# Kernel optimization log

Measured on AMD Instinct MI355X. Metric: run time of the kernel, lower is better.

## Reference

```python
import jax, jax.numpy as jnp
import numpy as np

N_NODES = 10000
N_EDGES = 100000
F_NODE = 128
F_EDGE = 16
HEADS = 8
OUT_CH = 128  # per-head channels in PyG TransformerConv
HC = HEADS * OUT_CH


def setup_inputs() -> dict:
    key = jax.random.key(0)
    ks = jax.random.split(key, 12)
    sN = 1.0 / np.sqrt(F_NODE)
    sE = 1.0 / np.sqrt(F_EDGE)
    return {
        "x": jax.random.normal(ks[0], (N_NODES, F_NODE), dtype=jnp.float32),
        "edge_attr": jax.random.normal(ks[1], (N_EDGES, F_EDGE), dtype=jnp.float32),
        "edge_index": jax.random.randint(ks[2], (2, N_EDGES), 0, N_NODES, dtype=jnp.int32),
        "Wq": jax.random.normal(ks[3], (F_NODE, HC), dtype=jnp.float32) * sN,
        "bq": jnp.zeros((HC,), dtype=jnp.float32),
        "Wk": jax.random.normal(ks[4], (F_NODE, HC), dtype=jnp.float32) * sN,
        "bk": jnp.zeros((HC,), dtype=jnp.float32),
        "Wv": jax.random.normal(ks[5], (F_NODE, HC), dtype=jnp.float32) * sN,
        "bv": jnp.zeros((HC,), dtype=jnp.float32),
        "We": jax.random.normal(ks[6], (F_EDGE, HC), dtype=jnp.float32) * sE,  # lin_edge has no bias in PyG
        "Wskip": jax.random.normal(ks[7], (F_NODE, OUT_CH), dtype=jnp.float32) * sN,
        "bskip": jnp.zeros((OUT_CH,), dtype=jnp.float32),
        "Wd": jax.random.normal(ks[8], (OUT_CH, 1), dtype=jnp.float32) * (1.0 / np.sqrt(OUT_CH)),
        "bd": jnp.zeros((1,), dtype=jnp.float32),
    }


def reference(x, edge_attr, edge_index, Wq, bq, Wk, bk, Wv, bv, We, Wskip, bskip, Wd, bd):
    N = x.shape[0]
    src, dst = edge_index[0], edge_index[1]  # messages flow src -> dst

    q = (x @ Wq + bq).reshape(N, HEADS, OUT_CH)
    k = (x @ Wk + bk).reshape(N, HEADS, OUT_CH)
    v = (x @ Wv + bv).reshape(N, HEADS, OUT_CH)
    e = (edge_attr @ We).reshape(-1, HEADS, OUT_CH)  # [E, H, C]

    k_j = k[src] + e                        # [E, H, C]
    alpha = jnp.einsum("ehc,ehc->eh", q[dst], k_j) / np.sqrt(OUT_CH)  # [E, H]

    # segment softmax over destination node
    m = jax.ops.segment_max(alpha, dst, num_segments=N)   # [N, H]
    a = jnp.exp(alpha - m[dst])
    s = jax.ops.segment_sum(a, dst, num_segments=N)       # [N, H]
    alpha_n = a / (s[dst] + 1e-16)                        # [E, H]

    msg = (v[src] + e) * alpha_n[:, :, None]              # [E, H, C]
    out = jax.ops.segment_sum(msg, dst, num_segments=N)   # [N, H, C]

    out = out.mean(axis=1)                                # concat=False -> head average, [N, C]
    out = out + x @ Wskip + bskip                         # root/skip connection
    out = jax.nn.relu(out)
    # dropout is identity at inference
    pooled = out.sum(axis=0)                              # [C]
    return pooled @ Wd + bd                               # [1]
```

## Files before the change

### kernel.cpp

```cpp
#include <hip/hip_runtime.h>

#define N_NODES 10000
#define N_EDGES 100000
#define F_NODE 128
#define HEADS 8
#define HC 1024
#define NCOLS2 2432
#define NB2 (NCOLS2 / 128)
#define SLOT_CAP 48

typedef __attribute__((ext_vector_type(8))) short bf16x8;
typedef __attribute__((ext_vector_type(4))) float f32x4;
typedef __attribute__((ext_vector_type(2))) float f32x2;

__device__ __forceinline__ void atomAddF(float* p, float v) {
    unsafeAtomicAdd(p, v);
}
__device__ __forceinline__ unsigned short f2bf(float f) {
    union { float f; unsigned u; } c; c.f = f;
    unsigned u = c.u + 0x7fffu + ((c.u >> 16) & 1u);
    return (unsigned short)(u >> 16);
}
__device__ __forceinline__ float bLo(unsigned x) {
    union { unsigned u; float f; } c; c.u = x << 16; return c.f;
}
__device__ __forceinline__ float bHi(unsigned x) {
    union { unsigned u; float f; } c; c.u = x & 0xffff0000u; return c.f;
}
__device__ __forceinline__ float bf2f(unsigned short u) {
    union { unsigned u; float f; } c; c.u = ((unsigned)u) << 16; return c.f;
}
__device__ __forceinline__ unsigned pk4fp8(unsigned a, unsigned b) {
    int w = __builtin_amdgcn_cvt_pk_fp8_f32(bLo(a), bHi(a), 0, false);
    w = __builtin_amdgcn_cvt_pk_fp8_f32(bLo(b), bHi(b), w, true);
    return (unsigned)w;
}
__device__ __forceinline__ void dq16v(uint4 q, f32x2* f) {
    f[0] = __builtin_amdgcn_cvt_pk_f32_fp8(q.x, false);
    f[1] = __builtin_amdgcn_cvt_pk_f32_fp8(q.x, true);
    f[2] = __builtin_amdgcn_cvt_pk_f32_fp8(q.y, false);
    f[3] = __builtin_amdgcn_cvt_pk_f32_fp8(q.y, true);
    f[4] = __builtin_amdgcn_cvt_pk_f32_fp8(q.z, false);
    f[5] = __builtin_amdgcn_cvt_pk_f32_fp8(q.z, true);
    f[6] = __builtin_amdgcn_cvt_pk_f32_fp8(q.w, false);
    f[7] = __builtin_amdgcn_cvt_pk_f32_fp8(q.w, true);
}
__device__ __forceinline__ void edge_accum2(
    uint4 xq4, uint4 vq4, float2 eav, float svv, bool valid,
    const f32x2* gf2, float qwx, float qwy, float du_r, float scale,
    float& s_reg, float& t0, float& t1, f32x2* va2) {
    f32x2 dac;
    dac.x = eav.x * qwx;
    dac.y = eav.y * qwy;
    f32x2 p;
    p = __builtin_amdgcn_cvt_pk_f32_fp8(xq4.x, false); dac += gf2[0] * p;
    p = __builtin_amdgcn_cvt_pk_f32_fp8(xq4.x, true);  dac += gf2[1] * p;
    p = __builtin_amdgcn_cvt_pk_f32_fp8(xq4.y, false); dac += gf2[2] * p;
    p = __builtin_amdgcn_cvt_pk_f32_fp8(xq4.y, true);  dac += gf2[3] * p;
    p = __builtin_amdgcn_cvt_pk_f32_fp8(xq4.z, false); dac += gf2[4] * p;
    p = __builtin_amdgcn_cvt_pk_f32_fp8(xq4.z, true);  dac += gf2[5] * p;
    p = __builtin_amdgcn_cvt_pk_f32_fp8(xq4.w, false); dac += gf2[6] * p;
    p = __builtin_amdgcn_cvt_pk_f32_fp8(xq4.w, true);  dac += gf2[7] * p;
    float d = dac.x + dac.y;
    d += __shfl_xor(d, 1); d += __shfl_xor(d, 2); d += __shfl_xor(d, 4);
    float a = __expf((d + du_r + svv) * scale);
    a = valid ? a : 0.f;
    s_reg += a;
    t0 += a * eav.x; t1 += a * eav.y;
    f32x2 av; av.x = a; av.y = a;
    p = __builtin_amdgcn_cvt_pk_f32_fp8(vq4.x, false); va2[0] += av * p;
    p = __builtin_amdgcn_cvt_pk_f32_fp8(vq4.x, true);  va2[1] += av * p;
    p = __builtin_amdgcn_cvt_pk_f32_fp8(vq4.y, false); va2[2] += av * p;
    p = __builtin_amdgcn_cvt_pk_f32_fp8(vq4.y, true);  va2[3] += av * p;
    p = __builtin_amdgcn_cvt_pk_f32_fp8(vq4.z, false); va2[4] += av * p;
    p = __builtin_amdgcn_cvt_pk_f32_fp8(vq4.z, true);  va2[5] += av * p;
    p = __builtin_amdgcn_cvt_pk_f32_fp8(vq4.w, false); va2[6] += av * p;
    p = __builtin_amdgcn_cvt_pk_f32_fp8(vq4.w, true);  va2[7] += av * p;
}

#define PREP_A 1250
#define PREP_B (PREP_A + NCOLS2 / 2)
#define PREP_C (PREP_B + 10)
#define PREP_D (PREP_C + 64)
__global__ __launch_bounds__(256) void prep_all(
    const float* __restrict__ x, unsigned short* __restrict__ xb,
    unsigned* __restrict__ xf8, const int* __restrict__ ei,
    int* __restrict__ cnt, int2* __restrict__ slots,
    const float* __restrict__ Wq, const float* __restrict__ Wk,
    const float* __restrict__ Wv, const float* __restrict__ Wskip,
    const float* __restrict__ We, const float* __restrict__ bq,
    const float* __restrict__ bk, const float* __restrict__ bv,
    const float* __restrict__ bskip, unsigned short* __restrict__ wt,
    float* __restrict__ bias, unsigned short* __restrict__ w2t) {
    __shared__ float wesh[2][128];
    __shared__ float wqsh[64][129];
    int tid = threadIdx.x;
    if (blockIdx.x < PREP_A) {
        int i = blockIdx.x * 256 + tid;
        float4 f = ((const float4*)x)[i];
        ushort4 o;
        o.x = f2bf(f.x); o.y = f2bf(f.y); o.z = f2bf(f.z); o.w = f2bf(f.w);
        ((ushort4*)xb)[i] = o;
        int w = __builtin_amdgcn_cvt_pk_fp8_f32(f.x, f.y, 0, false);
        w = __builtin_amdgcn_cvt_pk_fp8_f32(f.z, f.w, w, true);
        xf8[i] = (unsigned)w;
        if (i < N_EDGES) {
            int src = ei[i];
            int dst = ei[N_EDGES + i];
            int pos = atomicAdd(&cnt[dst], 1);
            if (pos < SLOT_CAP) slots[(size_t)dst * SLOT_CAP + pos] = make_int2(src, i);
        }
    } else if (blockIdx.x < PREP_B) {
        int bi = blockIdx.x - PREP_A;
        int cid = tid >> 7, d = tid & 127;
        int n = 2 * bi + cid;
        bool panel = (n < 1024) || (n >= 2176 && n < 2304);
        if (panel) {
            int h = (n < 1024) ? (n >> 7) : ((n - 2176) >> 4);
            if (n < 1024) {
                int f2 = n & 127;
                wesh[cid][d] = Wk[(size_t)f2 * HC + h * 128 + d];
            } else {
                int f = (n - 2176) & 15;
                wesh[cid][d] = We[(size_t)f * HC + h * 128 + d];
            }
            float s = 0.f;
            int c_t = tid & 63, r_t = tid >> 6;
            #pragma unroll 2
            for (int half = 0; half < 2; ++half) {
                #pragma unroll
                for (int rr = 0; rr < 32; ++rr) {
                    int r = rr * 4 + r_t;
                    wqsh[c_t][r] = Wq[(size_t)r * HC + h * 128 + half * 64 + c_t];
                }
                __syncthreads();
                #pragma unroll 16
                for (int cc = 0; cc < 64; ++cc)
                    s += wqsh[cc][d] * wesh[cid][half * 64 + cc];
                __syncthreads();
            }
            wt[(size_t)n * 128 + d] = f2bf(s);
        } else {
            float val;
            if (n < 2048) {
                val = Wv[(size_t)d * HC + (n - 1024)];
            } else if (n < 2176) {
                val = Wskip[(size_t)d * 128 + (n - 2048)];
            } else if (n < 2312) {
                int h = n - 2304;
                wesh[cid][d] = bk[h * 128 + d];
                __syncthreads();
                const float* wq = Wq + (size_t)d * HC + h * 128;
                float s = 0.f;
                #pragma unroll
                for (int c = 0; c < 128; ++c) s += wq[c] * wesh[cid][c];
                val = s;
            } else if (n < 2320) {
                int h = n - 2312;
                wesh[cid][d] = bq[h * 128 + d];
                __syncthreads();
                const float* wk = Wk + (size_t)d * HC + h * 128;
                float s = 0.f;
                #pragma unroll
                for (int c = 0; c < 128; ++c) s += wk[c] * wesh[cid][c];
                val = s;
            } else {
                val = 0.f;
            }
            wt[(size_t)n * 128 + d] = f2bf(val);
        }
    } else if (blockIdx.x < PREP_C) {
        int n = (blockIdx.x - PREP_B) * 256 + tid;
        if (n >= NCOLS2) return;
        float val;
        if (n < 1024) val = 0.f;
        else if (n < 2048) val = bv[n - 1024];
        else if (n < 2176) val = bskip[n - 2048];
        else if (n < 2304) {
            int hf = n - 2176, h = hf >> 4, f = hf & 15;
            float s = 0.f;
            for (int c = 0; c < 128; ++c)
                s += bq[h * 128 + c] * We[(size_t)f * HC + h * 128 + c];
            val = s;
        } else if (n < 2312) {
            int h = n - 2304;
            float s = 0.f;
            for (int c = 0; c < 128; ++c) s += bq[h * 128 + c] * bk[h * 128 + c];
            val = s;
        } else val = 0.f;
        bias[n] = val;
    } else {
        int c = (blockIdx.x - PREP_C) * 2 + (tid >> 7);
        int d = tid & 127;
        int h = d >> 4, f = d & 15;
        w2t[(size_t)c * 128 + d] = f2bf(We[(size_t)f * HC + h * 128 + c] * 0.125f);
    }
}

__global__ __launch_bounds__(256) void gemm_mfma(
    const unsigned short* __restrict__ xb, const unsigned short* __restrict__ wt,
    const float* __restrict__ bias, unsigned char* __restrict__ xgf8,
    unsigned char* __restrict__ vf8, unsigned short* __restrict__ sqb,
    float* __restrict__ du, float* __restrict__ sv) {
    __shared__ unsigned short lds[32768];
    unsigned short* ldsA = lds;
    unsigned short* ldsB = lds + 16384;
    int tid = threadIdx.x;
    int n0 = blockIdx.x * 128, m0 = blockIdx.y * 128;
    int w = tid >> 6, lane = tid & 63;
    int wm = (w >> 1) * 64, wn = (w & 1) * 64;
    int quad = lane >> 4, l16 = lane & 15;

    #pragma unroll
    for (int j = 0; j < 8; ++j) {
        int idx = j * 256 + tid;
        int kg = idx >> 7, r = idx & 127;
        unsigned short* dstA = ldsA + (size_t)(j * 256 + w * 64) * 8;
        __builtin_amdgcn_global_load_lds(
            (const unsigned int*)(xb + (size_t)(m0 + r) * 128 + kg * 8),
            (unsigned int*)dstA, 16, 0, 0);
    }
    #pragma unroll
    for (int j = 0; j < 8; ++j) {
        int idx = j * 256 + tid;
        int kg = idx >> 7, r = idx & 127;
        unsigned short* dstB = ldsB + (size_t)(j * 256 + w * 64) * 8;
        __builtin_amdgcn_global_load_lds(
            (const unsigned int*)(wt + (size_t)(n0 + r) * 128 + kg * 8),
            (unsigned int*)dstB, 16, 0, 0);
    }
    __syncthreads();

    f32x4 acc[4][4];
    #pragma unroll
    for (int i = 0; i < 4; ++i)
        #pragma unroll
        for (int j = 0; j < 4; ++j) acc[i][j] = (f32x4){0.f, 0.f, 0.f, 0.f};

    #pragma unroll
    for (int ks = 0; ks < 128; ks += 32) {
        int kb = (ks >> 3) + quad;
        bf16x8 a[4], b[4];
        #pragma unroll
        for (int mt = 0; mt < 4; ++mt)
            a[mt] = *(const bf16x8*)(ldsA + (size_t)kb * 1024 + (wm + mt * 16 + l16) * 8);
        #pragma unroll
        for (int nt = 0; nt < 4; ++nt)
            b[nt] = *(const bf16x8*)(ldsB + (size_t)kb * 1024 + (wn + nt * 16 + l16) * 8);
        #pragma unroll
        for (int mt = 0; mt < 4; ++mt)
            #pragma unroll
            for (int nt = 0; nt < 4; ++nt)
                acc[mt][nt] = __builtin_amdgcn_mfma_f32_16x16x32_bf16(
                    a[mt], b[nt], acc[mt][nt], 0, 0, 0);
    }
    __syncthreads();

    int nt0 = n0 >> 7;
    if (nt0 >= 16) {
        #pragma unroll
        for (int mt = 0; mt < 4; ++mt)
            #pragma unroll
            for (int r = 0; r < 4; ++r) {
                int row = m0 + wm + mt * 16 + quad * 4 + r;
                if (row >= N_NODES) continue;
                #pragma unroll
                for (int nt = 0; nt < 4; ++nt) {
                    int col = n0 + wn + nt * 16 + l16;
                    float val = acc[mt][nt][r] + bias[col];
                    if (col < 2304) {
                        sqb[(size_t)row * 256 + (col - 2048)] = f2bf(val);
                    } else if (col < 2312) {
                        du[(size_t)row * 8 + (col - 2304)] = val;
                    } else if (col < 2320) {
                        sv[(size_t)row * 8 + (col - 2312)] = val;
                    }
                }
            }
    } else {
        unsigned short* wst = lds + w * 4608;
        #pragma unroll
        for (int mt = 0; mt < 4; ++mt)
            #pragma unroll
            for (int r = 0; r < 4; ++r) {
                int rl = mt * 16 + quad * 4 + r;
                #pragma unroll
                for (int nt = 0; nt < 4; ++nt) {
                    int cl = nt * 16 + l16;
                    wst[rl * 72 + cl] = f2bf(acc[mt][nt][r] + bias[n0 + wn + cl]);
                }
            }
        unsigned char* dst = (nt0 < 8) ? xgf8 : vf8;
        int colbase = (n0 & 1023) + wn;
        #pragma unroll
        for (int p = 0; p < 4; ++p) {
            int rl = p * 16 + (lane >> 2);
            int row = m0 + wm + rl;
            if (row < N_NODES) {
                const uint4* sp = (const uint4*)(wst + rl * 72 + (lane & 3) * 16);
                uint4 u0 = sp[0], u1 = sp[1];
                uint4 o;
                o.x = pk4fp8(u0.x, u0.y);
                o.y = pk4fp8(u0.z, u0.w);
                o.z = pk4fp8(u1.x, u1.y);
                o.w = pk4fp8(u1.z, u1.w);
                *(uint4*)(dst + (size_t)row * 1024 + colbase + (lane & 3) * 16) = o;
            }
        }
    }
}

__global__ __launch_bounds__(256) void node_kernel(
    const unsigned char* __restrict__ xgf8, const unsigned char* __restrict__ xf8,
    const unsigned char* __restrict__ vf8, const unsigned short* __restrict__ sqb,
    const float* __restrict__ ea, const float* __restrict__ du,
    const float* __restrict__ sv, const int2* __restrict__ slots,
    const int* __restrict__ cnt, unsigned short* __restrict__ ttb,
    float* __restrict__ hsum) {
    int t = threadIdx.x;
    int w = t >> 6, lane = t & 63;
    int lh = lane & 7, h = lane >> 3;
    const float scale = 0.08838834764831845f;
    int n = __builtin_amdgcn_readfirstlane(blockIdx.x * 4 + w);

    uint4 gq = *(const uint4*)(xgf8 + (size_t)n * 1024 + 16 * lane);
    f32x2 gf2[8];
    dq16v(gq, gf2);
    ushort2 qwu = *(const ushort2*)(sqb + (size_t)n * 256 + 128 + h * 16 + 2 * lh);
    float qwx = bf2f(qwu.x), qwy = bf2f(qwu.y);
    float du_r = du[(size_t)n * 8 + h];

    int cn = cnt[n];
    cn = (cn > SLOT_CAP) ? SLOT_CAP : cn;
    cn = __builtin_amdgcn_readfirstlane(cn);
    const int2* sp = slots + (size_t)n * SLOT_CAP;
    const unsigned char* eab = (const unsigned char*)ea;

    unsigned xoff = lh * 16u;
    unsigned voff = lane * 16u;
    unsigned eoff = lh * 8u;

    f32x2 va2[8];
    #pragma unroll
    for (int i = 0; i < 8; ++i) va2[i] = (f32x2){0.f, 0.f};
    float s_reg = 0.f, t0 = 0.f, t1 = 0.f;

    if (cn > 0) {
        int np = (cn + 1) >> 1;
        uint4 x0A = {}, x0B = {}, v0A = {}, v0B = {};
        uint4 x1A = {}, x1B = {}, v1A = {}, v1B = {};
        float2 e0A = {}, e0B = {}, e1A = {}, e1B = {};
        float sv0A = 0.f, sv0B = 0.f, sv1A = 0.f, sv1B = 0.f;
        bool m0B = false, m1B = false;

#define LOADP(xA, xB, vA, vB, eA, eB, svA, svB, mB, pp) do {                    \
        int _p = (pp);                                                          \
        if (_p < np) {                                                          \
            int _i0 = 2 * _p;                                                   \
            bool _mb = (_i0 + 1) < cn;                                          \
            int2 _sa = sp[_i0];                                                 \
            int2 _sb = sp[_mb ? _i0 + 1 : _i0];                                 \
            mB = _mb;                                                           \
            xA = *(const uint4*)(xf8 + (((unsigned)_sa.x) << 7) + xoff);        \
            xB = *(const uint4*)(xf8 + (((unsigned)_sb.x) << 7) + xoff);        \
            vA = *(const uint4*)(vf8 + (((unsigned)_sa.x) << 10) + voff);       \
            vB = *(const uint4*)(vf8 + (((unsigned)_sb.x) << 10) + voff);       \
            eA = *(const float2*)(eab + (((unsigned)_sa.y) << 6) + eoff);       \
            eB = *(const float2*)(eab + (((unsigned)_sb.y) << 6) + eoff);       \
            svA = sv[(((unsigned)_sa.x) << 3) + h];                             \
            svB = sv[(((unsigned)_sb.x) << 3) + h];                             \
        }                                                                       \
    } while (0)

        LOADP(x0A, x0B, v0A, v0B, e0A, e0B, sv0A, sv0B, m0B, 0);
        LOADP(x1A, x1B, v1A, v1B, e1A, e1B, sv1A, sv1B, m1B, 1);
        int p = 0;
        while (true) {
            if (p >= np) break;
            edge_accum2(x0A, v0A, e0A, sv0A, true, gf2, qwx, qwy, du_r, scale,
                        s_reg, t0, t1, va2);
            edge_accum2(x0B, v0B, e0B, sv0B, m0B, gf2, qwx, qwy, du_r, scale,
                        s_reg, t0, t1, va2);
            LOADP(x0A, x0B, v0A, v0B, e0A, e0B, sv0A, sv0B, m0B, p + 2);
            ++p;
            if (p >= np) break;
            edge_accum2(x1A, v1A, e1A, sv1A, true, gf2, qwx, qwy, du_r, scale,
                        s_reg, t0, t1, va2);
            edge_accum2(x1B, v1B, e1B, sv1B, m1B, gf2, qwx, qwy, du_r, scale,
                        s_reg, t0, t1, va2);
            LOADP(x1A, x1B, v1A, v1B, e1A, e1B, sv1A, sv1B, m1B, p + 2);
            ++p;
        }
#undef LOADP
    }

    float inv = 1.f / (s_reg + 1e-16f);
    ushort2 tw;
    tw.x = f2bf(t0 * inv);
    tw.y = f2bf(t1 * inv);
    *(ushort2*)(ttb + (size_t)n * 128 + h * 16 + 2 * lh) = tw;
    float sc = inv * 0.125f;
    float va[16];
    #pragma unroll
    for (int i = 0; i < 8; ++i) { va[2 * i] = va2[i].x; va[2 * i + 1] = va2[i].y; }
    #pragma unroll
    for (int i = 0; i < 16; ++i) {
        float o = va[i] * sc;
        o += __shfl_xor(o, 8);
        o += __shfl_xor(o, 16);
        o += __shfl_xor(o, 32);
        va[i] = o;
    }
    if (lane < 8) {
        float* hp = hsum + (size_t)n * 128 + lane * 16;
        #pragma unroll
        for (int p2 = 0; p2 < 4; ++p2) {
            float4 h4 = make_float4(va[4 * p2], va[4 * p2 + 1],
                                    va[4 * p2 + 2], va[4 * p2 + 3]);
            ((float4*)hp)[p2] = h4;
        }
    }
}

__global__ __launch_bounds__(256) void out_gemm(
    const unsigned short* __restrict__ ttb, const unsigned short* __restrict__ w2t,
    const float* __restrict__ hsum, const unsigned short* __restrict__ sqb,
    float* __restrict__ pooled, int* __restrict__ done,
    const float* __restrict__ Wd, const float* __restrict__ bd,
    float* __restrict__ out) {
    __shared__ unsigned short As[64][136];
    __shared__ float pool_sh[128];
    __shared__ int last_sh;
    int tid = threadIdx.x;
    int m0 = blockIdx.x * 64;
    int w = tid >> 6, lane = tid & 63;
    int wm = (w >> 1) * 32, wn = (w & 1) * 64;
    int quad = lane >> 4, l16 = lane & 15;
    if (tid < 128) pool_sh[tid] = 0.f;
    #pragma unroll
    for (int tI = 0; tI < 4; ++tI) {
        int cId = tid + tI * 256;
        int r = cId >> 4, c8 = (cId & 15) << 3;
        int gr = m0 + r;
        uint4 av = make_uint4(0u, 0u, 0u, 0u);
        if (gr < N_NODES)
            av = *(const uint4*)(ttb + (size_t)gr * 128 + c8);
        *(uint4*)(&As[r][c8]) = av;
    }
    __syncthreads();
    f32x4 acc[2][4];
    #pragma unroll
    for (int i = 0; i < 2; ++i)
        #pragma unroll
        for (int j = 0; j < 4; ++j) acc[i][j] = (f32x4){0.f, 0.f, 0.f, 0.f};

    const unsigned short* bb = w2t + (size_t)(wn + l16) * 128 + quad * 8;
    #pragma unroll
    for (int ks = 0; ks < 128; ks += 32) {
        bf16x8 a[2], b[4];
        #pragma unroll
        for (int mt = 0; mt < 2; ++mt)
            a[mt] = *(const bf16x8*)&As[wm + mt * 16 + l16][ks + quad * 8];
        #pragma unroll
        for (int nt = 0; nt < 4; ++nt)
            b[nt] = *(const bf16x8*)(bb + (size_t)nt * 16 * 128 + ks);
        #pragma unroll
        for (int mt = 0; mt < 2; ++mt)
            #pragma unroll
            for (int nt = 0; nt < 4; ++nt)
                acc[mt][nt] = __builtin_amdgcn_mfma_f32_16x16x32_bf16(
                    a[mt], b[nt], acc[mt][nt], 0, 0, 0);
    }
    float pl[4] = {0.f, 0.f, 0.f, 0.f};
    #pragma unroll
    for (int mt = 0; mt < 2; ++mt) {
        #pragma unroll
        for (int r = 0; r < 4; ++r) {
            int row = m0 + wm + mt * 16 + quad * 4 + r;
            if (row >= N_NODES) continue;
            #pragma unroll
            for (int nt = 0; nt < 4; ++nt) {
                int col = wn + nt * 16 + l16;
                float val = acc[mt][nt][r] + hsum[(size_t)row * 128 + col]
                            + bf2f(sqb[(size_t)row * 256 + col]);
                pl[nt] += fmaxf(val, 0.f);
            }
        }
    }
    #pragma unroll
    for (int nt = 0; nt < 4; ++nt)
        atomicAdd(&pool_sh[wn + nt * 16 + l16], pl[nt]);
    __syncthreads();
    if (tid < 128) atomAddF(&pooled[tid], pool_sh[tid]);
    __threadfence();
    if (tid == 0) last_sh = (atomicAdd(done, 1) == (int)gridDim.x - 1);
    __syncthreads();
    if (last_sh && tid < 64) {
        float p0 = __hip_atomic_load(&pooled[2 * tid], __ATOMIC_RELAXED,
                                     __HIP_MEMORY_SCOPE_AGENT);
        float p1 = __hip_atomic_load(&pooled[2 * tid + 1], __ATOMIC_RELAXED,
                                     __HIP_MEMORY_SCOPE_AGENT);
        float vv = p0 * Wd[2 * tid] + p1 * Wd[2 * tid + 1];
        vv += __shfl_xor(vv, 1);  vv += __shfl_xor(vv, 2);  vv += __shfl_xor(vv, 4);
        vv += __shfl_xor(vv, 8);  vv += __shfl_xor(vv, 16); vv += __shfl_xor(vv, 32);
        if (tid == 0) out[0] = vv + bd[0];
    }
}

extern "C" void kernel_launch(void* const* d_in, const int* in_sizes, int n_in,
                              void* d_out, int out_size, void* d_ws, size_t ws_size,
                              hipStream_t stream) {
    const float* x     = (const float*)d_in[0];
    const float* eattr = (const float*)d_in[1];
    const int*   ei    = (const int*)d_in[2];
    const float* Wq    = (const float*)d_in[3];
    const float* bq    = (const float*)d_in[4];
    const float* Wk    = (const float*)d_in[5];
    const float* bk    = (const float*)d_in[6];
    const float* Wv    = (const float*)d_in[7];
    const float* bv    = (const float*)d_in[8];
    const float* We    = (const float*)d_in[9];
    const float* Wskip = (const float*)d_in[10];
    const float* bskip = (const float*)d_in[11];
    const float* Wd    = (const float*)d_in[12];
    const float* bd    = (const float*)d_in[13];
    float* out = (float*)d_out;

    char* ws = (char*)d_ws;
    unsigned char*  xgf8 = (unsigned char*)(ws + 0);
    unsigned char*  vf8  = (unsigned char*)(ws + 10240000);
    unsigned short* sqb  = (unsigned short*)(ws + 20480000);
    float* hsum = (float*)(ws + 25600000);
    unsigned short* xb   = (unsigned short*)(ws + 30720000);
    unsigned short* ttb  = xb;
    unsigned*       xf8  = (unsigned*)(ws + 33280000);
    float* du   = (float*)(ws + 34560000);
    float* sv   = (float*)(ws + 34880000);
    unsigned short* wt   = (unsigned short*)(ws + 35200000);
    float* bias = (float*)(ws + 35822592);
    unsigned short* w2t  = (unsigned short*)(ws + 35832320);
    int* cnt    = (int*)(ws + 35865088);
    float* pooled = (float*)(ws + 35905088);
    int* done   = (int*)(ws + 35905600);
    int2* slots = (int2*)(ws + 35905616);

    hipMemsetAsync(cnt, 0, 40000 + 512 + 16, stream);

    prep_all<<<PREP_D, 256, 0, stream>>>(
        x, xb, xf8, ei, cnt, slots, Wq, Wk, Wv, Wskip, We, bq, bk, bv, bskip,
        wt, bias, w2t);

    gemm_mfma<<<dim3(NB2, (N_NODES + 127) / 128), 256, 0, stream>>>(
        xb, wt, bias, xgf8, vf8, sqb, du, sv);

    node_kernel<<<N_NODES / 4, 256, 0, stream>>>(
        xgf8, (const unsigned char*)xf8, vf8, sqb, eattr, du, sv, slots, cnt,
        ttb, hsum);

    out_gemm<<<(N_NODES + 63) / 64, 256, 0, stream>>>(
        ttb, w2t, hsum, sqb, pooled, done, Wd, bd, out);
}
```

Before: 179.6 us.

## Fuse output projection and pooling into node kernel, drop out_gemm launch

Removes the separate out_gemm kernel. The node kernel now keeps per-node attention results in LDS and computes the 128x128 projection, skip add, relu and pooling itself with scalar FMAs against a bf16 weight tile copied into LDS. Pooled atomics are spread over 64 partial buffers to reduce contention, and the last block reduces them. This saves a launch plus the global round trip for ttb/hsum, but every block now loads 34KB of weights into LDS, which may reduce occupancy, and it trades MFMA for scalar FMA work.

```diff
diff --git a/kernel.cpp b/kernel.cpp
--- a/kernel.cpp
+++ b/kernel.cpp
@@ -8,6 +8,7 @@
 #define NCOLS2 2432
 #define NB2 (NCOLS2 / 128)
 #define SLOT_CAP 48
+#define NPOOL 64
 
 typedef __attribute__((ext_vector_type(8))) short bf16x8;
 typedef __attribute__((ext_vector_type(4))) float f32x4;
@@ -315,13 +316,28 @@
     const unsigned char* __restrict__ vf8, const unsigned short* __restrict__ sqb,
     const float* __restrict__ ea, const float* __restrict__ du,
     const float* __restrict__ sv, const int2* __restrict__ slots,
-    const int* __restrict__ cnt, unsigned short* __restrict__ ttb,
-    float* __restrict__ hsum) {
+    const int* __restrict__ cnt, const unsigned short* __restrict__ w2t,
+    float* __restrict__ pooled, int* __restrict__ done,
+    const float* __restrict__ Wd, const float* __restrict__ bd,
+    float* __restrict__ out) {
+    __shared__ alignas(16) unsigned short w2sh[128][136];
+    __shared__ alignas(16) unsigned short t_lds[4][128];
+    __shared__ alignas(16) float h_lds[4][128];
+    __shared__ float pool_sh[128];
+    __shared__ int last_sh;
     int t = threadIdx.x;
     int w = t >> 6, lane = t & 63;
     int lh = lane & 7, h = lane >> 3;
     const float scale = 0.08838834764831845f;
     int n = __builtin_amdgcn_readfirstlane(blockIdx.x * 4 + w);
+
+    #pragma unroll
+    for (int j = 0; j < 8; ++j) {
+        int c = t + j * 256;
+        int r = c >> 4, k16 = c & 15;
+        *(uint4*)(&w2sh[r][k16 * 8]) = *(const uint4*)(w2t + (size_t)r * 128 + k16 * 8);
+    }
+    if (t < 128) pool_sh[t] = 0.f;
 
     uint4 gq = *(const uint4*)(xgf8 + (size_t)n * 1024 + 16 * lane);
     f32x2 gf2[8];
@@ -398,7 +414,7 @@
     ushort2 tw;
     tw.x = f2bf(t0 * inv);
     tw.y = f2bf(t1 * inv);
-    *(ushort2*)(ttb + (size_t)n * 128 + h * 16 + 2 * lh) = tw;
+    *(ushort2*)(&t_lds[w][h * 16 + 2 * lh]) = tw;
     float sc = inv * 0.125f;
     float va[16];
     #pragma unroll
@@ -412,98 +428,59 @@
         va[i] = o;
     }
     if (lane < 8) {
-        float* hp = hsum + (size_t)n * 128 + lane * 16;
         #pragma unroll
         for (int p2 = 0; p2 < 4; ++p2) {
             float4 h4 = make_float4(va[4 * p2], va[4 * p2 + 1],
                                     va[4 * p2 + 2], va[4 * p2 + 3]);
-            ((float4*)hp)[p2] = h4;
-        }
-    }
-}
-
-__global__ __launch_bounds__(256) void out_gemm(
-    const unsigned short* __restrict__ ttb, const unsigned short* __restrict__ w2t,
-    const float* __restrict__ hsum, const unsigned short* __restrict__ sqb,
-    float* __restrict__ pooled, int* __restrict__ done,
-    const float* __restrict__ Wd, const float* __restrict__ bd,
-    float* __restrict__ out) {
-    __shared__ unsigned short As[64][136];
-    __shared__ float pool_sh[128];
-    __shared__ int last_sh;
-    int tid = threadIdx.x;
-    int m0 = blockIdx.x * 64;
-    int w = tid >> 6, lane = tid & 63;
-    int wm = (w >> 1) * 32, wn = (w & 1) * 64;
-    int quad = lane >> 4, l16 = lane & 15;
-    if (tid < 128) pool_sh[tid] = 0.f;
-    #pragma unroll
-    for (int tI = 0; tI < 4; ++tI) {
-        int cId = tid + tI * 256;
-        int r = cId >> 4, c8 = (cId & 15) << 3;
-        int gr = m0 + r;
-        uint4 av = make_uint4(0u, 0u, 0u, 0u);
-        if (gr < N_NODES)
-            av = *(const uint4*)(ttb + (size_t)gr * 128 + c8);
-        *(uint4*)(&As[r][c8]) = av;
+            *(float4*)(&h_lds[w][lane * 16 + p2 * 4]) = h4;
+        }
     }
     __syncthreads();
-    f32x4 acc[2][4];
-    #pragma unroll
-    for (int i = 0; i < 2; ++i)
-        #pragma unroll
-        for (int j = 0; j < 4; ++j) acc[i][j] = (f32x4){0.f, 0.f, 0.f, 0.f};
-
-    const unsigned short* bb = w2t + (size_t)(wn + l16) * 128 + quad * 8;
-    #pragma unroll
-    for (int ks = 0; ks < 128; ks += 32) {
-        bf16x8 a[2], b[4];
-        #pragma unroll
-        for (int mt = 0; mt < 2; ++mt)
-            a[mt] = *(const bf16x8*)&As[wm + mt * 16 + l16][ks + quad * 8];
-        #pragma unroll
-        for (int nt = 0; nt < 4; ++nt)
-            b[nt] = *(const bf16x8*)(bb + (size_t)nt * 16 * 128 + ks);
-        #pragma unroll
-        for (int mt = 0; mt < 2; ++mt)
-            #pragma unroll
-            for (int nt = 0; nt < 4; ++nt)
-                acc[mt][nt] = __builtin_amdgcn_mfma_f32_16x16x32_bf16(
-                    a[mt], b[nt], acc[mt][nt], 0, 0, 0);
-    }
-    float pl[4] = {0.f, 0.f, 0.f, 0.f};
-    #pragma unroll
-    for (int mt = 0; mt < 2; ++mt) {
-        #pragma unroll
-        for (int r = 0; r < 4; ++r) {
-            int row = m0 + wm + mt * 16 + quad * 4 + r;
-            if (row >= N_NODES) continue;
-            #pragma unroll
-            for (int nt = 0; nt < 4; ++nt) {
-                int col = wn + nt * 16 + l16;
-                float val = acc[mt][nt][r] + hsum[(size_t)row * 128 + col]
-                            + bf2f(sqb[(size_t)row * 256 + col]);
-                pl[nt] += fmaxf(val, 0.f);
-            }
-        }
-    }
-    #pragma unroll
-    for (int nt = 0; nt < 4; ++nt)
-        atomicAdd(&pool_sh[wn + nt * 16 + l16], pl[nt]);
+
+    {
+        const unsigned short* trow = t_lds[w];
+        const unsigned short* w0p = &w2sh[lane][0];
+        const unsigned short* w1p = &w2sh[lane + 64][0];
+        float o0 = h_lds[w][lane]      + bf2f(sqb[(size_t)n * 256 + lane]);
+        float o1 = h_lds[w][lane + 64] + bf2f(sqb[(size_t)n * 256 + lane + 64]);
+        #pragma unroll
+        for (int k8 = 0; k8 < 16; ++k8) {
+            uint4 tq = *(const uint4*)(trow + k8 * 8);
+            uint4 a0 = *(const uint4*)(w0p + k8 * 8);
+            uint4 a1 = *(const uint4*)(w1p + k8 * 8);
+            o0 += bLo(tq.x) * bLo(a0.x) + bHi(tq.x) * bHi(a0.x);
+            o1 += bLo(tq.x) * bLo(a1.x) + bHi(tq.x) * bHi(a1.x);
+            o0 += bLo(tq.y) * bLo(a0.y) + bHi(tq.y) * bHi(a0.y);
+            o1 += bLo(tq.y) * bLo(a1.y) + bHi(tq.y) * bHi(a1.y);
+            o0 += bLo(tq.z) * bLo(a0.z) + bHi(tq.z) * bHi(a0.z);
+            o1 += bLo(tq.z) * bLo(a1.z) + bHi(tq.z) * bHi(a1.z);
+            o0 += bLo(tq.w) * bLo(a0.w) + bHi(tq.w) * bHi(a0.w);
+            o1 += bLo(tq.w) * bLo(a1.w) + bHi(tq.w) * bHi(a1.w);
+        }
+        atomicAdd(&pool_sh[lane], fmaxf(o0, 0.f));
+        atomicAdd(&pool_sh[lane + 64], fmaxf(o1, 0.f));
+    }
     __syncthreads();
-    if (tid < 128) atomAddF(&pooled[tid], pool_sh[tid]);
+    if (t < 128)
+        atomAddF(&pooled[(size_t)(blockIdx.x & (NPOOL - 1)) * 128 + t], pool_sh[t]);
     __threadfence();
-    if (tid == 0) last_sh = (atomicAdd(done, 1) == (int)gridDim.x - 1);
+    if (t == 0) last_sh = (atomicAdd(done, 1) == (int)gridDim.x - 1);
     __syncthreads();
-    if (last_sh && tid < 64) {
-        float p0 = __hip_atomic_load(&pooled[2 * tid], __ATOMIC_RELAXED,
-                                     __HIP_MEMORY_SCOPE_AGENT);
-        float p1 = __hip_atomic_load(&pooled[2 * tid + 1], __ATOMIC_RELAXED,
-                                     __HIP_MEMORY_SCOPE_AGENT);
-        float vv = p0 * Wd[2 * tid] + p1 * Wd[2 * tid + 1];
-        vv += __shfl_xor(vv, 1);  vv += __shfl_xor(vv, 2);  vv += __shfl_xor(vv, 4);
-        vv += __shfl_xor(vv, 8);  vv += __shfl_xor(vv, 16); vv += __shfl_xor(vv, 32);
-        if (tid == 0) out[0] = vv + bd[0];
+    if (last_sh) {
+        if (t < 128) {
+            float s = 0.f;
+            for (int r = 0; r < NPOOL; ++r)
+                s += __hip_atomic_load(&pooled[(size_t)r * 128 + t],
+                                       __ATOMIC_RELAXED, __HIP_MEMORY_SCOPE_AGENT);
+            pool_sh[t] = s;
+        }
+        __syncthreads();
+        if (t < 64) {
+            float vv = pool_sh[2 * t] * Wd[2 * t] + pool_sh[2 * t + 1] * Wd[2 * t + 1];
+            vv += __shfl_xor(vv, 1);  vv += __shfl_xor(vv, 2);  vv += __shfl_xor(vv, 4);
+            vv += __shfl_xor(vv, 8);  vv += __shfl_xor(vv, 16); vv += __shfl_xor(vv, 32);
+            if (t == 0) out[0] = vv + bd[0];
+        }
     }
 }
 
@@ -530,9 +507,8 @@
     unsigned char*  xgf8 = (unsigned char*)(ws + 0);
     unsigned char*  vf8  = (unsigned char*)(ws + 10240000);
     unsigned short* sqb  = (unsigned short*)(ws + 20480000);
-    float* hsum = (float*)(ws + 25600000);
+    float* pooled2 = (float*)(ws + 25600000);
     unsigned short* xb   = (unsigned short*)(ws + 30720000);
-    unsigned short* ttb  = xb;
     unsigned*       xf8  = (unsigned*)(ws + 33280000);
     float* du   = (float*)(ws + 34560000);
     float* sv   = (float*)(ws + 34880000);
@@ -540,11 +516,11 @@
     float* bias = (float*)(ws + 35822592);
     unsigned short* w2t  = (unsigned short*)(ws + 35832320);
     int* cnt    = (int*)(ws + 35865088);
-    float* pooled = (float*)(ws + 35905088);
     int* done   = (int*)(ws + 35905600);
     int2* slots = (int2*)(ws + 35905616);
 
     hipMemsetAsync(cnt, 0, 40000 + 512 + 16, stream);
+    hipMemsetAsync(pooled2, 0, NPOOL * 128 * 4, stream);
 
     prep_all<<<PREP_D, 256, 0, stream>>>(
         x, xb, xf8, ei, cnt, slots, Wq, Wk, Wv, Wskip, We, bq, bk, bv, bskip,
@@ -555,8 +531,5 @@
 
     node_kernel<<<N_NODES / 4, 256, 0, stream>>>(
         xgf8, (const unsigned char*)xf8, vf8, sqb, eattr, du, sv, slots, cnt,
-        ttb, hsum);
-
-    out_gemm<<<(N_NODES + 63) / 64, 256, 0, stream>>>(
-        ttb, w2t, hsum, sqb, pooled, done, Wd, bd, out);
-}
+        w2t, pooled2, done, Wd, bd, out);
+}
```

Result: slower. 357.5 us (+99.0%).
